# Kernel optimization log

Hardware: AMD Instinct MI355X
Metric: run time of the kernel (lower is better)

The kernel has to match this reference:

```python
import jax, jax.numpy as jnp
import numpy as np

N = 100000   # nodes
E = 1600000  # edges
DF = 256     # dim_features
H = 64       # hidden (layers=[64,64])
T = 4        # dim_target
G = 8        # graphs in batch
BN_EPS = 1e-5


def setup_inputs() -> dict:
    key = jax.random.key(0)
    ks = jax.random.split(key, 16)
    x = jax.random.normal(ks[0], (N, DF), jnp.float32)
    edge_index = jax.random.randint(ks[1], (2, E), 0, N)
    batch = jnp.sort(jax.random.randint(ks[2], (N,), 0, G))

    def lin(k, fan_in, fan_out):
        return jax.random.normal(k, (fan_in, fan_out), jnp.float32) / np.sqrt(fan_in)

    return {
        "x": x,
        "edge_index": edge_index,
        "batch": batch,
        # first_h: Linear(DF,H)+BN+ReLU
        "W_first": lin(ks[3], DF, H),
        "b_first": jnp.zeros((H,), jnp.float32),
        "bn1_g": jnp.ones((H,), jnp.float32),
        "bn1_b": jnp.zeros((H,), jnp.float32),
        # linears[0]: Linear(H,T)
        "W_lin0": lin(ks[4], H, T),
        "b_lin0": jnp.zeros((T,), jnp.float32),
        # GINConv nn: Linear(H,H)+BN+ReLU
        "W_conv": lin(ks[5], H, H),
        "b_conv": jnp.zeros((H,), jnp.float32),
        "bn2_g": jnp.ones((H,), jnp.float32),
        "bn2_b": jnp.zeros((H,), jnp.float32),
        # linears[1]: Linear(H,T)
        "W_lin1": lin(ks[6], H, T),
        "b_lin1": jnp.zeros((T,), jnp.float32),
    }


def _bn(h, gamma, beta):
    # BatchNorm1d in training mode: batch statistics over node dim
    mu = h.mean(axis=0)
    var = h.var(axis=0)
    return gamma * (h - mu) / jnp.sqrt(var + BN_EPS) + beta


def reference(x, edge_index, batch,
              W_first, b_first, bn1_g, bn1_b,
              W_lin0, b_lin0,
              W_conv, b_conv, bn2_g, bn2_b,
              W_lin1, b_lin1):
    # Layer 0: first_h = Linear+BN+ReLU
    f = jax.nn.relu(_bn(x @ W_first + b_first, bn1_g, bn1_b))  # [N,H]
    np0 = f @ W_lin0 + b_lin0                                  # [N,T]
    node_pred = np0
    wsi_pred = jax.ops.segment_max(np0, batch, num_segments=G)  # global_max_pool

    # Layer 1: GINConv (eps=0): nn(x_i + sum_{j->i} x_j)
    src, dst = edge_index[0], edge_index[1]
    agg = jax.ops.segment_sum(f[src], dst, num_segments=N)     # [N,H]
    h = f + agg
    f = jax.nn.relu(_bn(h @ W_conv + b_conv, bn2_g, bn2_b))    # [N,H]
    np1 = f @ W_lin1 + b_lin1                                  # [N,T]
    node_pred = node_pred + np1
    wsi_pred = wsi_pred + jax.ops.segment_max(np1, batch, num_segments=G)

    return wsi_pred, node_pred
```

## Files before the change

### kernel.cpp

```cpp
#include <hip/hip_runtime.h>
#include <math.h>

#define NN 100000
#define NE 1600000
#define DF 256
#define HH 64
#define TT 4
#define GG 8
#define BN_EPS 1e-5f
#define NTOT (NE + NN)

#define BROWS 512
#define NBK ((NN + BROWS - 1) / BROWS)
#define BCAP 10240
#define PCHUNK 1600
#define NPB (NE / PCHUNK)

typedef __attribute__((ext_vector_type(8))) short short8v;
typedef __attribute__((ext_vector_type(4))) float f32x4;
typedef unsigned short ushort_t;
typedef unsigned int uint_t;

__device__ __forceinline__ void atomicMaxF(float* addr, float val) {
  if (val >= 0.f) atomicMax((int*)addr, __float_as_int(val));
  else            atomicMin((unsigned int*)addr, __float_as_uint(val));
}

__device__ __forceinline__ short f2bf(float f) {
  uint_t u = __float_as_uint(f);
  u += 0x7FFFu + ((u >> 16) & 1u);
  return (short)(u >> 16);
}
__device__ __forceinline__ float bf2f(uint_t u) { return __uint_as_float(u << 16); }
__device__ __forceinline__ float bfhi(uint_t u) { return __uint_as_float(u & 0xFFFF0000u); }

__global__ void k_setup(const float* __restrict__ Wf, ushort_t* __restrict__ Wbf,
                        const float* __restrict__ Wc, ushort_t* __restrict__ Wbf2,
                        float* __restrict__ stats, float* __restrict__ maxb,
                        int* __restrict__ Bcnt) {
  int i = blockIdx.x * 256 + threadIdx.x;
  if (i < DF * HH) Wbf[i] = (ushort_t)f2bf(Wf[i]);
  else {
    int j = i - DF * HH;
    if (j < HH * HH) Wbf2[j] = (ushort_t)f2bf(Wc[j]);
  }
  if (i < 512) stats[i] = 0.f;
  if (i < 64)  maxb[i]  = -INFINITY;
  if (i < NBK) Bcnt[i]  = 0;
}

__global__ __launch_bounds__(256, 2) void k_gemm1_mfma(
    const float* __restrict__ x, const ushort_t* __restrict__ Wbf,
    const float* __restrict__ b, ushort_t* __restrict__ h1,
    float* __restrict__ stats) {
  const int lane = threadIdx.x & 63;
  const int li = lane & 15;
  const int lh = lane >> 4;
  const int gw = (blockIdx.x * 256 + (int)threadIdx.x) >> 6;
  const int nw = (gridDim.x * 256) >> 6;

  short8v bf[8][4];
#pragma unroll
  for (int s = 0; s < 8; ++s)
#pragma unroll
    for (int ct = 0; ct < 4; ++ct)
#pragma unroll
      for (int e = 0; e < 8; ++e)
        bf[s][ct][e] = (short)Wbf[(32 * s + 8 * lh + e) * HH + ct * 16 + li];

  float bias[4];
#pragma unroll
  for (int ct = 0; ct < 4; ++ct) bias[ct] = b[ct * 16 + li];

  float ps[4] = {0.f, 0.f, 0.f, 0.f}, pss[4] = {0.f, 0.f, 0.f, 0.f};

  for (int t = gw; t < NN / 16; t += nw) {
    const float* xb = x + (size_t)(t * 16 + li) * DF + 8 * lh;
    f32x4 acc[4];
#pragma unroll
    for (int ct = 0; ct < 4; ++ct) acc[ct] = (f32x4){0.f, 0.f, 0.f, 0.f};

#pragma unroll
    for (int s = 0; s < 8; ++s) {
      float4 a0 = *(const float4*)(xb + 32 * s);
      float4 a1 = *(const float4*)(xb + 32 * s + 4);
      short8v af;
      af[0] = f2bf(a0.x); af[1] = f2bf(a0.y); af[2] = f2bf(a0.z); af[3] = f2bf(a0.w);
      af[4] = f2bf(a1.x); af[5] = f2bf(a1.y); af[6] = f2bf(a1.z); af[7] = f2bf(a1.w);
#pragma unroll
      for (int ct = 0; ct < 4; ++ct)
        acc[ct] = __builtin_amdgcn_mfma_f32_16x16x32_bf16(af, bf[s][ct], acc[ct], 0, 0, 0);
    }

    ushort_t* hb = h1 + (size_t)t * 16 * HH;
#pragma unroll
    for (int ct = 0; ct < 4; ++ct) {
#pragma unroll
      for (int r = 0; r < 4; ++r) {
        float h = acc[ct][r] + bias[ct];
        hb[(lh * 4 + r) * HH + ct * 16 + li] = (ushort_t)f2bf(h);
        ps[ct] += h; pss[ct] += h * h;
      }
    }
  }

#pragma unroll
  for (int ct = 0; ct < 4; ++ct) {
    ps[ct]  += __shfl_xor(ps[ct], 16);  ps[ct]  += __shfl_xor(ps[ct], 32);
    pss[ct] += __shfl_xor(pss[ct], 16); pss[ct] += __shfl_xor(pss[ct], 32);
  }
  if (lane < 16) {
#pragma unroll
    for (int ct = 0; ct < 4; ++ct) {
      atomicAdd(&stats[ct * 16 + lane], ps[ct]);
      atomicAdd(&stats[HH + ct * 16 + lane], pss[ct]);
    }
  }
}

__global__ void k_finalize_bn(const float* __restrict__ sums,
                              const float* __restrict__ gamma,
                              const float* __restrict__ beta,
                              float* __restrict__ ab) {
  int c = threadIdx.x;
  float mu  = sums[c] * (1.f / NN);
  float var = sums[HH + c] * (1.f / NN) - mu * mu;
  float a = gamma[c] * rsqrtf(var + BN_EPS);
  ab[c] = a;
  ab[HH + c] = beta[c] - mu * a;
}

__global__ __launch_bounds__(256) void k_norm_gemm2(
    const ushort_t* __restrict__ h1, const float* __restrict__ ab,
    const float* __restrict__ Wl0, const float* __restrict__ bl0,
    const int* __restrict__ batch, const ushort_t* __restrict__ Wbf2,
    float* __restrict__ node_pred, float* __restrict__ maxbuf,
    ushort_t* __restrict__ g) {
  __shared__ float lmax[GG * TT];
  if (threadIdx.x < GG * TT) lmax[threadIdx.x] = -INFINITY;
  __syncthreads();

  const int lane = threadIdx.x & 63;
  const int li = lane & 15;
  const int lh = lane >> 4;
  const int gw = (blockIdx.x * 256 + (int)threadIdx.x) >> 6;
  const int nw = (gridDim.x * 256) >> 6;

  short8v bfr[2][4];
#pragma unroll
  for (int s = 0; s < 2; ++s)
#pragma unroll
    for (int ct = 0; ct < 4; ++ct)
#pragma unroll
      for (int e = 0; e < 8; ++e)
        bfr[s][ct][e] = (short)Wbf2[(32 * s + 8 * lh + e) * HH + ct * 16 + li];

  short8v bhd[2];
#pragma unroll
  for (int s = 0; s < 2; ++s)
#pragma unroll
    for (int e = 0; e < 8; ++e)
      bhd[s][e] = (li < TT) ? f2bf(Wl0[(32 * s + 8 * lh + e) * TT + li]) : (short)0;

  const float4 sa0 = *(const float4*)(ab + 8 * lh);
  const float4 sa1 = *(const float4*)(ab + 8 * lh + 4);
  const float4 sb0 = *(const float4*)(ab + HH + 8 * lh);
  const float4 sb1 = *(const float4*)(ab + HH + 8 * lh + 4);
  const float4 ta0 = *(const float4*)(ab + 32 + 8 * lh);
  const float4 ta1 = *(const float4*)(ab + 32 + 8 * lh + 4);
  const float4 tb0 = *(const float4*)(ab + HH + 32 + 8 * lh);
  const float4 tb1 = *(const float4*)(ab + HH + 32 + 8 * lh + 4);
  const float blv = (li < TT) ? bl0[li] : 0.f;

  for (int t = gw; t < NN / 16; t += nw) {
    const ushort_t* hb = h1 + (size_t)(t * 16 + li) * HH + 8 * lh;
    uint4 xa = *(const uint4*)(hb);
    uint4 xc = *(const uint4*)(hb + 32);

    short8v af0, af1;
    af0[0] = f2bf(fmaxf(fmaf(sa0.x, bf2f(xa.x), sb0.x), 0.f));
    af0[1] = f2bf(fmaxf(fmaf(sa0.y, bfhi(xa.x), sb0.y), 0.f));
    af0[2] = f2bf(fmaxf(fmaf(sa0.z, bf2f(xa.y), sb0.z), 0.f));
    af0[3] = f2bf(fmaxf(fmaf(sa0.w, bfhi(xa.y), sb0.w), 0.f));
    af0[4] = f2bf(fmaxf(fmaf(sa1.x, bf2f(xa.z), sb1.x), 0.f));
    af0[5] = f2bf(fmaxf(fmaf(sa1.y, bfhi(xa.z), sb1.y), 0.f));
    af0[6] = f2bf(fmaxf(fmaf(sa1.z, bf2f(xa.w), sb1.z), 0.f));
    af0[7] = f2bf(fmaxf(fmaf(sa1.w, bfhi(xa.w), sb1.w), 0.f));
    af1[0] = f2bf(fmaxf(fmaf(ta0.x, bf2f(xc.x), tb0.x), 0.f));
    af1[1] = f2bf(fmaxf(fmaf(ta0.y, bfhi(xc.x), tb0.y), 0.f));
    af1[2] = f2bf(fmaxf(fmaf(ta0.z, bf2f(xc.y), tb0.z), 0.f));
    af1[3] = f2bf(fmaxf(fmaf(ta0.w, bfhi(xc.y), tb0.w), 0.f));
    af1[4] = f2bf(fmaxf(fmaf(ta1.x, bf2f(xc.z), tb1.x), 0.f));
    af1[5] = f2bf(fmaxf(fmaf(ta1.y, bfhi(xc.z), tb1.y), 0.f));
    af1[6] = f2bf(fmaxf(fmaf(ta1.z, bf2f(xc.w), tb1.z), 0.f));
    af1[7] = f2bf(fmaxf(fmaf(ta1.w, bfhi(xc.w), tb1.w), 0.f));

    f32x4 acc[4], acch;
#pragma unroll
    for (int ct = 0; ct < 4; ++ct) {
      acc[ct] = (f32x4){0.f, 0.f, 0.f, 0.f};
      acc[ct] = __builtin_amdgcn_mfma_f32_16x16x32_bf16(af0, bfr[0][ct], acc[ct], 0, 0, 0);
      acc[ct] = __builtin_amdgcn_mfma_f32_16x16x32_bf16(af1, bfr[1][ct], acc[ct], 0, 0, 0);
    }
    acch = (f32x4){0.f, 0.f, 0.f, 0.f};
    acch = __builtin_amdgcn_mfma_f32_16x16x32_bf16(af0, bhd[0], acch, 0, 0, 0);
    acch = __builtin_amdgcn_mfma_f32_16x16x32_bf16(af1, bhd[1], acch, 0, 0, 0);

    ushort_t* gb = g + (size_t)t * 16 * HH;
#pragma unroll
    for (int ct = 0; ct < 4; ++ct)
#pragma unroll
      for (int r = 0; r < 4; ++r)
        gb[(lh * 4 + r) * HH + ct * 16 + li] = (ushort_t)f2bf(acc[ct][r]);

    if (li < TT) {
#pragma unroll
      for (int r = 0; r < 4; ++r) {
        int row = t * 16 + lh * 4 + r;
        float np = acch[r] + blv;
        atomicMaxF(&lmax[batch[row] * TT + li], np);
        node_pred[(size_t)row * TT + li] = np;
      }
    }
  }
  __syncthreads();
  if (threadIdx.x < GG * TT) atomicMaxF(&maxbuf[threadIdx.x], lmax[threadIdx.x]);
}

__global__ __launch_bounds__(256) void k_norm_np(
    const ushort_t* __restrict__ hin,
    const float* __restrict__ ab, const float* __restrict__ Wlin,
    const float* __restrict__ blin, const int* __restrict__ batch,
    float* __restrict__ node_pred, float* __restrict__ maxbuf, int rpb) {
  __shared__ float lmax[GG * TT];
  if (threadIdx.x < GG * TT) lmax[threadIdx.x] = -INFINITY;
  __syncthreads();

  const int lane = threadIdx.x & 63;
  const int wid  = threadIdx.x >> 6;
  const float a  = ab[lane];
  const float b2 = ab[HH + lane];
  const float4 w = ((const float4*)Wlin)[lane];
  const float4 bl = *(const float4*)blin;
  int r0 = blockIdx.x * rpb;
  int r1 = min(r0 + rpb, NN);

  for (int r = r0 + wid; r < r1; r += 4) {
    float h = bf2f(hin[(size_t)r * HH + lane]);
    float f = fmaxf(fmaf(a, h, b2), 0.f);
    float p0 = f * w.x, p1 = f * w.y, p2 = f * w.z, p3 = f * w.w;
#pragma unroll
    for (int off = 32; off; off >>= 1) {
      p0 += __shfl_xor(p0, off);
      p1 += __shfl_xor(p1, off);
      p2 += __shfl_xor(p2, off);
      p3 += __shfl_xor(p3, off);
    }
    if (lane == 0) {
      float4 np;
      np.x = p0 + bl.x; np.y = p1 + bl.y; np.z = p2 + bl.z; np.w = p3 + bl.w;
      int g = batch[r];
      atomicMaxF(&lmax[g * TT + 0], np.x);
      atomicMaxF(&lmax[g * TT + 1], np.y);
      atomicMaxF(&lmax[g * TT + 2], np.z);
      atomicMaxF(&lmax[g * TT + 3], np.w);
      float4* op = (float4*)(node_pred + (size_t)r * TT);
      float4 o = *op;
      np.x += o.x; np.y += o.y; np.z += o.z; np.w += o.w;
      *op = np;
    }
  }
  __syncthreads();
  if (threadIdx.x < GG * TT) atomicMaxF(&maxbuf[threadIdx.x], lmax[threadIdx.x]);
}

__global__ __launch_bounds__(256) void k_part(
    const int* __restrict__ ei, int* __restrict__ Bcnt,
    uint2* __restrict__ ebuf) {
  __shared__ int hist[256], start[256], cnt[256], gbase[256];
  __shared__ int ssrc[PCHUNK], sdst[PCHUNK];
  const int t = threadIdx.x;
  hist[t] = 0; cnt[t] = 0;
  __syncthreads();
  const int e0 = blockIdx.x * PCHUNK;
  for (int i = t; i < PCHUNK; i += 256)
    atomicAdd(&hist[ei[NE + e0 + i] >> 9], 1);
  __syncthreads();
  int v = hist[t];
  start[t] = v;
  __syncthreads();
  for (int off = 1; off < 256; off <<= 1) {
    int u = (t >= off) ? start[t - off] : 0;
    __syncthreads();
    start[t] += u;
    __syncthreads();
  }
  int incl = start[t];
  __syncthreads();
  start[t] = incl - v;
  if (v > 0) gbase[t] = atomicAdd(&Bcnt[t], v);
  __syncthreads();
  for (int i = t; i < PCHUNK; i += 256) {
    int src = ei[e0 + i];
    int dst = ei[NE + e0 + i];
    int b = dst >> 9;
    int p = start[b] + atomicAdd(&cnt[b], 1);
    ssrc[p] = src; sdst[p] = dst;
  }
  __syncthreads();
  for (int i = t; i < PCHUNK; i += 256) {
    int dst = sdst[i];
    int b = dst >> 9;
    uint2 pr; pr.x = (uint_t)ssrc[i]; pr.y = (uint_t)dst;
    ebuf[(size_t)b * BCAP + gbase[b] + (i - start[b])] = pr;
  }
}

__global__ void k_bscan(const int* __restrict__ Bcnt, int* __restrict__ Bbase) {
  __shared__ int s[256];
  int t = threadIdx.x;
  int v = 0;
  if (t < NBK) {
    int rows = min(BROWS, NN - t * BROWS);
    v = Bcnt[t] + rows;
  }
  s[t] = v;
  __syncthreads();
  for (int off = 1; off < 256; off <<= 1) {
    int u = (t >= off) ? s[t - off] : 0;
    __syncthreads();
    s[t] += u;
    __syncthreads();
  }
  if (t < NBK) Bbase[t] = s[t] - v;
}

__global__ __launch_bounds__(256) void k_fill2(
    const int* __restrict__ Bcnt, const int* __restrict__ Bbase,
    const uint2* __restrict__ ebuf, int* __restrict__ rowstart,
    int* __restrict__ srcl) {
  __shared__ int cnt[BROWS];
  __shared__ int ssum[256];
  const int b = blockIdx.x;
  const int r0 = b * BROWS;
  const int nrows = min(BROWS, NN - r0);
  const int ne = Bcnt[b];
  const int base = Bbase[b];
  const uint2* eb = ebuf + (size_t)b * BCAP;
  const int t = threadIdx.x;

  cnt[2 * t] = (2 * t < nrows) ? 1 : 0;
  cnt[2 * t + 1] = (2 * t + 1 < nrows) ? 1 : 0;
  __syncthreads();
  for (int j = t; j < ne; j += 256)
    atomicAdd(&cnt[(int)eb[j].y - r0], 1);
  __syncthreads();

  int a0 = cnt[2 * t], a1 = cnt[2 * t + 1];
  ssum[t] = a0 + a1;
  __syncthreads();
  for (int off = 1; off < 256; off <<= 1) {
    int u = (t >= off) ? ssum[t - off] : 0;
    __syncthreads();
    ssum[t] += u;
    __syncthreads();
  }
  int e0 = base + ssum[t] - (a0 + a1);
  int e1 = e0 + a0;
  __syncthreads();
  if (2 * t < nrows)     { rowstart[r0 + 2 * t] = e0;     srcl[e0] = r0 + 2 * t; }
  if (2 * t + 1 < nrows) { rowstart[r0 + 2 * t + 1] = e1; srcl[e1] = r0 + 2 * t + 1; }
  cnt[2 * t] = e0 + 1;
  cnt[2 * t + 1] = e1 + 1;
  __syncthreads();
  for (int j = t; j < ne; j += 256) {
    uint2 pr = eb[j];
    int p = atomicAdd(&cnt[(int)pr.y - r0], 1);
    srcl[p] = (int)pr.x;
  }
}

#define RF(x) __builtin_amdgcn_readfirstlane(x)
#define GLD(V, I) asm volatile("global_load_ushort %0, %1, %2" \
    : "=v"(V) : "v"(voff), "s"(g + (size_t)(I) * HH) : "memory")
#define WAIT16 do { asm volatile("s_waitcnt vmcnt(16)" ::: "memory"); \
    __builtin_amdgcn_sched_barrier(0); } while (0)
#define WAIT0 do { asm volatile("s_waitcnt vmcnt(0)" ::: "memory"); \
    __builtin_amdgcn_sched_barrier(0); } while (0)
#define ISSUE16(P, EB) do { \
  int j0 = RF(srcl[(EB) + 0]),  j1 = RF(srcl[(EB) + 1]); \
  int j2 = RF(srcl[(EB) + 2]),  j3 = RF(srcl[(EB) + 3]); \
  int j4 = RF(srcl[(EB) + 4]),  j5 = RF(srcl[(EB) + 5]); \
  int j6 = RF(srcl[(EB) + 6]),  j7 = RF(srcl[(EB) + 7]); \
  int j8 = RF(srcl[(EB) + 8]),  j9 = RF(srcl[(EB) + 9]); \
  int j10 = RF(srcl[(EB) + 10]), j11 = RF(srcl[(EB) + 11]); \
  int j12 = RF(srcl[(EB) + 12]), j13 = RF(srcl[(EB) + 13]); \
  int j14 = RF(srcl[(EB) + 14]), j15 = RF(srcl[(EB) + 15]); \
  GLD(P##0, j0);  GLD(P##1, j1);  GLD(P##2, j2);  GLD(P##3, j3); \
  GLD(P##4, j4);  GLD(P##5, j5);  GLD(P##6, j6);  GLD(P##7, j7); \
  GLD(P##8, j8);  GLD(P##9, j9);  GLD(P##10, j10); GLD(P##11, j11); \
  GLD(P##12, j12); GLD(P##13, j13); GLD(P##14, j14); GLD(P##15, j15); \
} while (0)
#define CJ(V, EI) do { \
  if ((EI) == nb) { \
    h2[(size_t)cur * HH + lane] = (ushort_t)f2bf(acc); ps += acc; pss += acc * acc; \
    cur++; nb = __builtin_amdgcn_readlane(rsv, cur - wra); acc = bc; \
  } \
  acc += bf2f(V); } while (0)
#define CONS16(P, EB) do { \
  CJ(P##0, (EB) + 0);  CJ(P##1, (EB) + 1);  CJ(P##2, (EB) + 2);  CJ(P##3, (EB) + 3); \
  CJ(P##4, (EB) + 4);  CJ(P##5, (EB) + 5);  CJ(P##6, (EB) + 6);  CJ(P##7, (EB) + 7); \
  CJ(P##8, (EB) + 8);  CJ(P##9, (EB) + 9);  CJ(P##10, (EB) + 10); CJ(P##11, (EB) + 11); \
  CJ(P##12, (EB) + 12); CJ(P##13, (EB) + 13); CJ(P##14, (EB) + 14); CJ(P##15, (EB) + 15); \
} while (0)

__global__ __launch_bounds__(256) void k_gather(
    const ushort_t* __restrict__ g, const int* __restrict__ rowstart,
    const int* __restrict__ srcl, const float* __restrict__ bias,
    ushort_t* __restrict__ h2, float* __restrict__ stats) {
  const int lane = threadIdx.x & 63;
  const int wid  = threadIdx.x >> 6;
  const float bc = bias[lane];
  const uint_t voff = lane * 2;
  const int wra = (blockIdx.x * 4 + wid) * 8;

  int ridx = wra + 1 + lane;
  int rsv = (ridx < NN) ? rowstart[ridx] : NTOT;

  int e    = RF(rowstart[wra]);
  int eEnd = __builtin_amdgcn_readlane(rsv, 7);
  int cur  = wra;
  int nb   = __builtin_amdgcn_readlane(rsv, 0);
  float acc = bc, ps = 0.f, pss = 0.f;

  uint_t A0, A1, A2, A3, A4, A5, A6, A7, A8, A9, A10, A11, A12, A13, A14, A15;
  uint_t B0, B1, B2, B3, B4, B5, B6, B7, B8, B9, B10, B11, B12, B13, B14, B15;

  int n = (eEnd - e) >> 4;
  if (n > 0) {
    int pend = e;
    ISSUE16(A, e); e += 16; n--;
    while (n >= 2) {
      int eb = e;
      ISSUE16(B, e); e += 16; n--;
      WAIT16; CONS16(A, pend); pend = eb;
      int ea = e;
      ISSUE16(A, e); e += 16; n--;
      WAIT16; CONS16(B, pend); pend = ea;
    }
    if (n == 1) {
      int eb = e;
      ISSUE16(B, e); e += 16;
      WAIT16; CONS16(A, pend); pend = eb;
      WAIT0;  CONS16(B, pend);
    } else {
      WAIT0;  CONS16(A, pend);
    }
  }
  for (; e < eEnd; ++e) {
    if (e == nb) {
      h2[(size_t)cur * HH + lane] = (ushort_t)f2bf(acc); ps += acc; pss += acc * acc;
      cur++; nb = __builtin_amdgcn_readlane(rsv, cur - wra); acc = bc;
    }
    int i = RF(srcl[e]);
    acc += bf2f(g[(size_t)i * HH + lane]);
  }
  h2[(size_t)cur * HH + lane] = (ushort_t)f2bf(acc); ps += acc; pss += acc * acc;

  __shared__ float sred[4][128];
  sred[wid][lane] = ps;
  sred[wid][64 + lane] = pss;
  __syncthreads();
  if (wid == 0) {
    float s0 = sred[0][lane] + sred[1][lane] + sred[2][lane] + sred[3][lane];
    float q0 = sred[0][64 + lane] + sred[1][64 + lane] + sred[2][64 + lane] + sred[3][64 + lane];
    atomicAdd(&stats[lane], s0);
    atomicAdd(&stats[HH + lane], q0);
  }
}

__global__ void k_wsi(const float* __restrict__ m0, const float* __restrict__ m1,
                      float* __restrict__ out) {
  int i = threadIdx.x;
  out[i] = m0[i] + m1[i];
}

extern "C" void kernel_launch(void* const* d_in, const int* in_sizes, int n_in,
                              void* d_out, int out_size, void* d_ws, size_t ws_size,
                              hipStream_t stream) {
  const float* x    = (const float*)d_in[0];
  const int*   ei   = (const int*)d_in[1];
  const int*   bat  = (const int*)d_in[2];
  const float* Wf   = (const float*)d_in[3];
  const float* bf   = (const float*)d_in[4];
  const float* g1   = (const float*)d_in[5];
  const float* be1  = (const float*)d_in[6];
  const float* Wl0  = (const float*)d_in[7];
  const float* bl0  = (const float*)d_in[8];
  const float* Wc   = (const float*)d_in[9];
  const float* bc   = (const float*)d_in[10];
  const float* g2   = (const float*)d_in[11];
  const float* be2  = (const float*)d_in[12];
  const float* Wl1  = (const float*)d_in[13];
  const float* bl1  = (const float*)d_in[14];

  float* out   = (float*)d_out;
  float* wsi   = out;
  float* npred = out + GG * TT;

  ushort_t* h2bf   = (ushort_t*)d_ws;
  ushort_t* h1bf   = h2bf + (size_t)NN * HH;
  ushort_t* gbf    = h1bf + (size_t)NN * HH;
  float*    stats1 = (float*)(gbf + (size_t)NN * HH);
  float*    stats2 = stats1 + 256;
  float*    maxb   = stats2 + 256;
  int*      rowstart = (int*)(maxb + 64);
  int*      Bcnt     = rowstart + NN;
  int*      Bbase    = Bcnt + 256;
  int*      srcl     = Bbase + 256;
  uint2*    ebuf     = (uint2*)(srcl + NTOT);
  ushort_t* Wbf      = (ushort_t*)(ebuf + (size_t)NBK * BCAP);
  ushort_t* Wbf2     = Wbf + DF * HH;

  k_setup<<<dim3(80), dim3(256), 0, stream>>>(Wf, Wbf, Wc, Wbf2, stats1, maxb, Bcnt);
  k_part<<<dim3(NPB), dim3(256), 0, stream>>>(ei, Bcnt, ebuf);
  k_bscan<<<dim3(1), dim3(256), 0, stream>>>(Bcnt, Bbase);
  k_fill2<<<dim3(NBK), dim3(256), 0, stream>>>(Bcnt, Bbase, ebuf, rowstart, srcl);

  k_gemm1_mfma<<<dim3(512), dim3(256), 0, stream>>>(x, Wbf, bf, h1bf, stats1);
  k_finalize_bn<<<dim3(1), dim3(64), 0, stream>>>(stats1, g1, be1, stats1 + 128);
  k_norm_gemm2<<<dim3(512), dim3(256), 0, stream>>>(
      h1bf, stats1 + 128, Wl0, bl0, bat, Wbf2, npred, maxb, gbf);

  k_gather<<<dim3(NN / 32), dim3(256), 0, stream>>>(
      gbf, rowstart, srcl, bc, h2bf, stats2);
  k_finalize_bn<<<dim3(1), dim3(64), 0, stream>>>(stats2, g2, be2, stats2 + 128);
  k_norm_np<<<dim3(512), dim3(256), 0, stream>>>(
      h2bf, stats2 + 128, Wl1, bl1, bat, npred, maxb + 32, (NN + 511) / 512);

  k_wsi<<<dim3(1), dim3(32), 0, stream>>>(maxb, maxb + 32, wsi);
}
```

Measured before the change: 299.7 us.

## Stage GEMM1 weights in LDS, fold BN finalize into consumer kernels

Moves the first GEMM's bf16 weight fragments from a 128-register per-thread array into a 32 KB shared-memory table. This frees registers, so the 2-waves launch bound is dropped and the grid is doubled to 1024 blocks for more latency hiding on the streaming x reads. It also removes both single-block k_finalize_bn launches by having each consumer block compute the BN scale and shift into shared memory. The cost is LDS reads inside the MFMA loop and redundant per-block finalize work.

Measured after the change: 344.4 us. 1.15x slower.

```diff
diff --git a/kernel.cpp b/kernel.cpp
--- a/kernel.cpp
+++ b/kernel.cpp
@@ -49,24 +49,29 @@
   if (i < NBK) Bcnt[i]  = 0;
 }
 
-__global__ __launch_bounds__(256, 2) void k_gemm1_mfma(
+__global__ __launch_bounds__(256) void k_gemm1_mfma(
     const float* __restrict__ x, const ushort_t* __restrict__ Wbf,
     const float* __restrict__ b, ushort_t* __restrict__ h1,
     float* __restrict__ stats) {
+  __shared__ short8v Wf[32][64];
   const int lane = threadIdx.x & 63;
   const int li = lane & 15;
   const int lh = lane >> 4;
+
+  for (int i = threadIdx.x; i < 32 * 64; i += 256) {
+    int fi = i >> 6, le = i & 63;
+    int s = fi >> 2, ct = fi & 3;
+    int lli = le & 15, llh = le >> 4;
+    short8v v;
+#pragma unroll
+    for (int e = 0; e < 8; ++e)
+      v[e] = (short)Wbf[(32 * s + 8 * llh + e) * HH + ct * 16 + lli];
+    Wf[fi][le] = v;
+  }
+  __syncthreads();
+
   const int gw = (blockIdx.x * 256 + (int)threadIdx.x) >> 6;
   const int nw = (gridDim.x * 256) >> 6;
-
-  short8v bf[8][4];
-#pragma unroll
-  for (int s = 0; s < 8; ++s)
-#pragma unroll
-    for (int ct = 0; ct < 4; ++ct)
-#pragma unroll
-      for (int e = 0; e < 8; ++e)
-        bf[s][ct][e] = (short)Wbf[(32 * s + 8 * lh + e) * HH + ct * 16 + li];
 
   float bias[4];
 #pragma unroll
@@ -89,7 +94,7 @@
       af[4] = f2bf(a1.x); af[5] = f2bf(a1.y); af[6] = f2bf(a1.z); af[7] = f2bf(a1.w);
 #pragma unroll
       for (int ct = 0; ct < 4; ++ct)
-        acc[ct] = __builtin_amdgcn_mfma_f32_16x16x32_bf16(af, bf[s][ct], acc[ct], 0, 0, 0);
+        acc[ct] = __builtin_amdgcn_mfma_f32_16x16x32_bf16(af, Wf[4 * s + ct][lane], acc[ct], 0, 0, 0);
     }
 
     ushort_t* hb = h1 + (size_t)t * 16 * HH;
@@ -118,26 +123,24 @@
   }
 }
 
-__global__ void k_finalize_bn(const float* __restrict__ sums,
-                              const float* __restrict__ gamma,
-                              const float* __restrict__ beta,
-                              float* __restrict__ ab) {
-  int c = threadIdx.x;
-  float mu  = sums[c] * (1.f / NN);
-  float var = sums[HH + c] * (1.f / NN) - mu * mu;
-  float a = gamma[c] * rsqrtf(var + BN_EPS);
-  ab[c] = a;
-  ab[HH + c] = beta[c] - mu * a;
-}
-
 __global__ __launch_bounds__(256) void k_norm_gemm2(
-    const ushort_t* __restrict__ h1, const float* __restrict__ ab,
+    const ushort_t* __restrict__ h1, const float* __restrict__ stats,
+    const float* __restrict__ gamma, const float* __restrict__ beta,
     const float* __restrict__ Wl0, const float* __restrict__ bl0,
     const int* __restrict__ batch, const ushort_t* __restrict__ Wbf2,
     float* __restrict__ node_pred, float* __restrict__ maxbuf,
     ushort_t* __restrict__ g) {
   __shared__ float lmax[GG * TT];
+  __shared__ float abl[128];
   if (threadIdx.x < GG * TT) lmax[threadIdx.x] = -INFINITY;
+  if (threadIdx.x < 64) {
+    int c = threadIdx.x;
+    float mu  = stats[c] * (1.f / NN);
+    float var = stats[HH + c] * (1.f / NN) - mu * mu;
+    float a = gamma[c] * rsqrtf(var + BN_EPS);
+    abl[c] = a;
+    abl[HH + c] = beta[c] - mu * a;
+  }
   __syncthreads();
 
   const int lane = threadIdx.x & 63;
@@ -162,14 +165,14 @@
     for (int e = 0; e < 8; ++e)
       bhd[s][e] = (li < TT) ? f2bf(Wl0[(32 * s + 8 * lh + e) * TT + li]) : (short)0;
 
-  const float4 sa0 = *(const float4*)(ab + 8 * lh);
-  const float4 sa1 = *(const float4*)(ab + 8 * lh + 4);
-  const float4 sb0 = *(const float4*)(ab + HH + 8 * lh);
-  const float4 sb1 = *(const float4*)(ab + HH + 8 * lh + 4);
-  const float4 ta0 = *(const float4*)(ab + 32 + 8 * lh);
-  const float4 ta1 = *(const float4*)(ab + 32 + 8 * lh + 4);
-  const float4 tb0 = *(const float4*)(ab + HH + 32 + 8 * lh);
-  const float4 tb1 = *(const float4*)(ab + HH + 32 + 8 * lh + 4);
+  const float4 sa0 = *(const float4*)(abl + 8 * lh);
+  const float4 sa1 = *(const float4*)(abl + 8 * lh + 4);
+  const float4 sb0 = *(const float4*)(abl + HH + 8 * lh);
+  const float4 sb1 = *(const float4*)(abl + HH + 8 * lh + 4);
+  const float4 ta0 = *(const float4*)(abl + 32 + 8 * lh);
+  const float4 ta1 = *(const float4*)(abl + 32 + 8 * lh + 4);
+  const float4 tb0 = *(const float4*)(abl + HH + 32 + 8 * lh);
+  const float4 tb1 = *(const float4*)(abl + HH + 32 + 8 * lh + 4);
   const float blv = (li < TT) ? bl0[li] : 0.f;
 
   for (int t = gw; t < NN / 16; t += nw) {
@@ -228,18 +231,28 @@
 }
 
 __global__ __launch_bounds__(256) void k_norm_np(
-    const ushort_t* __restrict__ hin,
-    const float* __restrict__ ab, const float* __restrict__ Wlin,
-    const float* __restrict__ blin, const int* __restrict__ batch,
-    float* __restrict__ node_pred, float* __restrict__ maxbuf, int rpb) {
+    const ushort_t* __restrict__ hin, const float* __restrict__ stats,
+    const float* __restrict__ gamma, const float* __restrict__ beta,
+    const float* __restrict__ Wlin, const float* __restrict__ blin,
+    const int* __restrict__ batch, float* __restrict__ node_pred,
+    float* __restrict__ maxbuf, int rpb) {
   __shared__ float lmax[GG * TT];
+  __shared__ float abl[128];
   if (threadIdx.x < GG * TT) lmax[threadIdx.x] = -INFINITY;
+  if (threadIdx.x < 64) {
+    int c = threadIdx.x;
+    float mu  = stats[c] * (1.f / NN);
+    float var = stats[HH + c] * (1.f / NN) - mu * mu;
+    float a = gamma[c] * rsqrtf(var + BN_EPS);
+    abl[c] = a;
+    abl[HH + c] = beta[c] - mu * a;
+  }
   __syncthreads();
 
   const int lane = threadIdx.x & 63;
   const int wid  = threadIdx.x >> 6;
-  const float a  = ab[lane];
-  const float b2 = ab[HH + lane];
+  const float a  = abl[lane];
+  const float b2 = abl[HH + lane];
   const float4 w = ((const float4*)Wlin)[lane];
   const float4 bl = *(const float4*)blin;
   int r0 = blockIdx.x * rpb;
@@ -527,16 +540,14 @@
   k_bscan<<<dim3(1), dim3(256), 0, stream>>>(Bcnt, Bbase);
   k_fill2<<<dim3(NBK), dim3(256), 0, stream>>>(Bcnt, Bbase, ebuf, rowstart, srcl);
 
-  k_gemm1_mfma<<<dim3(512), dim3(256), 0, stream>>>(x, Wbf, bf, h1bf, stats1);
-  k_finalize_bn<<<dim3(1), dim3(64), 0, stream>>>(stats1, g1, be1, stats1 + 128);
+  k_gemm1_mfma<<<dim3(1024), dim3(256), 0, stream>>>(x, Wbf, bf, h1bf, stats1);
   k_norm_gemm2<<<dim3(512), dim3(256), 0, stream>>>(
-      h1bf, stats1 + 128, Wl0, bl0, bat, Wbf2, npred, maxb, gbf);
+      h1bf, stats1, g1, be1, Wl0, bl0, bat, Wbf2, npred, maxb, gbf);
 
   k_gather<<<dim3(NN / 32), dim3(256), 0, stream>>>(
       gbf, rowstart, srcl, bc, h2bf, stats2);
-  k_finalize_bn<<<dim3(1), dim3(64), 0, stream>>>(stats2, g2, be2, stats2 + 128);
   k_norm_np<<<dim3(512), dim3(256), 0, stream>>>(
-      h2bf, stats2 + 128, Wl1, bl1, bat, npred, maxb + 32, (NN + 511) / 512);
+      h2bf, stats2, g2, be2, Wl1, bl1, bat, npred, maxb + 32, (NN + 511) / 512);
 
   k_wsi<<<dim3(1), dim3(32), 0, stream>>>(maxb, maxb + 32, wsi);
 }
```
